# Performance work log

Measured on AMD Instinct MI355X. Metric: run time of the kernel, lower is better.

## Reference

```python
import jax, jax.numpy as jnp
import numpy as np

N_NODES = 32
GAT_OUT = 64
LSTM_H = 128
N_CLS = 4
NEG_SLOPE = 0.2


def setup_inputs() -> dict:
    key = jax.random.key(0)
    ks = jax.random.split(key, 12)
    B, T, E = 32, 512, 96
    F, H = GAT_OUT, LSTM_H
    s = 0.05
    return {
        "x_seq": jax.random.normal(ks[0], (B, T, N_NODES), jnp.float32),
        "edge_index": jax.random.randint(ks[1], (2, E), 0, N_NODES, jnp.int32),
        # GATConv params (heads=1): lin weight [in=1, F], attention vectors [F], bias [F]
        "w_gat": jax.random.normal(ks[2], (1, F), jnp.float32) * s,
        "att_src": jax.random.normal(ks[3], (F,), jnp.float32) * s,
        "att_dst": jax.random.normal(ks[4], (F,), jnp.float32) * s,
        "b_gat": jnp.zeros((F,), jnp.float32),
        # LSTM params, torch gate order (i, f, g, o)
        "W_ih": jax.random.normal(ks[5], (N_NODES * F, 4 * H), jnp.float32) * s,
        "W_hh": jax.random.normal(ks[6], (H, 4 * H), jnp.float32) * s,
        "b_ih": jnp.zeros((4 * H,), jnp.float32),
        "b_hh": jnp.zeros((4 * H,), jnp.float32),
        # classifier
        "W_fc": jax.random.normal(ks[7], (H, N_CLS), jnp.float32) * s,
        "b_fc": jnp.zeros((N_CLS,), jnp.float32),
    }


def _forward(x_seq, edge_index, w_gat, att_src, att_dst, b_gat,
             W_ih, W_hh, b_ih, b_hh, W_fc, b_fc):
    B, T, N = x_seq.shape
    F = w_gat.shape[1]
    H = W_hh.shape[0]

    # --- GAT over all (B,T) steps at once (PyG GATConv, heads=1, self-loops) ---
    loops = jnp.arange(N, dtype=edge_index.dtype)
    src = jnp.concatenate([edge_index[0], loops])  # [Et]
    dst = jnp.concatenate([edge_index[1], loops])  # [Et]
    Et = src.shape[0]

    h = x_seq[..., None] * w_gat            # [B,T,N,F] (in_channels=1 linear)
    a_s = h @ att_src                        # [B,T,N]
    a_d = h @ att_dst                        # [B,T,N]
    e = a_s[..., src] + a_d[..., dst]        # [B,T,Et]
    e = jnp.where(e > 0, e, NEG_SLOPE * e)   # LeakyReLU(0.2)

    # segment softmax over destination node, batched over B*T
    e2 = jnp.moveaxis(e, -1, 0).reshape(Et, B * T)
    m = jax.ops.segment_max(e2, dst, num_segments=N)        # [N,B*T]
    ex = jnp.exp(e2 - m[dst])
    z = jax.ops.segment_sum(ex, dst, num_segments=N)        # [N,B*T]
    alpha = ex / z[dst]                                      # [Et,B*T]
    alpha = jnp.moveaxis(alpha.reshape(Et, B, T), 0, -1)     # [B,T,Et]

    msg = alpha[..., None] * h[:, :, src, :]                 # [B,T,Et,F]
    onehot = (dst[:, None] == jnp.arange(N)).astype(h.dtype)  # [Et,N]
    out = jnp.einsum('btef,en->btnf', msg, onehot) + b_gat    # [B,T,N,F]

    seq = out.reshape(B, T, N * F)           # [B,T,2048]

    # --- single-layer LSTM (batch_first), torch gate order i,f,g,o ---
    xw = seq @ W_ih + (b_ih + b_hh)          # [B,T,4H]

    def step(carry, xw_t):
        hs, cs = carry
        g = xw_t + hs @ W_hh                 # [B,4H]
        i, f, gg, o = jnp.split(g, 4, axis=-1)
        cs = jax.nn.sigmoid(f) * cs + jax.nn.sigmoid(i) * jnp.tanh(gg)
        hs = jax.nn.sigmoid(o) * jnp.tanh(cs)
        return (hs, cs), None

    h0 = jnp.zeros((B, H), seq.dtype)
    (h_last, _), _ = jax.lax.scan(step, (h0, h0), jnp.moveaxis(xw, 1, 0))

    return h_last @ W_fc + b_fc              # [B,num_classes]


def reference(x_seq, edge_index, w_gat, att_src, att_dst, b_gat,
              W_ih, W_hh, b_ih, b_hh, W_fc, b_fc):
    return _forward(x_seq, edge_index, w_gat, att_src, att_dst, b_gat,
                    W_ih, W_hh, b_ih, b_hh, W_fc, b_fc)
```

## Files before the change

kernel.cpp:

```cpp
#include <hip/hip_runtime.h>
#include <hip/hip_fp16.h>

#define NN 32
#define FF 64
#define HH 128
#define G4 512
#define BB 32
#define TT 512
#define ET 128
#define NPOS (BB*TT)
#define POSB 32

__device__ __forceinline__ float frcp(float x) { return __builtin_amdgcn_rcpf(x); }

__global__ __launch_bounds__(512) void prep_kernel(const float* __restrict__ w_gat,
                                                   const float* __restrict__ b_gat,
                                                   const float* __restrict__ W_ih,
                                                   const float* __restrict__ W_hh,
                                                   float* __restrict__ W_eff,
                                                   float* __restrict__ biasp,
                                                   float* __restrict__ Wt) {
  int j = threadIdx.x;
  int n = blockIdx.x;
  float accw = 0.f, accb = 0.f;
#pragma unroll 8
  for (int f = 0; f < FF; ++f) {
    float wv = W_ih[(n * FF + f) * G4 + j];
    accw = fmaf(w_gat[f], wv, accw);
    accb = fmaf(b_gat[f], wv, accb);
  }
  W_eff[n * G4 + j] = accw;
  biasp[n * G4 + j] = accb;
  __half* Wt16 = (__half*)Wt;
  int g0 = (n * G4 + j) * 4;
#pragma unroll
  for (int qq = 0; qq < 4; ++qq) {
    int E = g0 + qq;
    int tl = E >> 7;
    int idx = E & 127;
    int frag = idx >> 3;
    int e = idx & 7;
    int g = frag >> 2, q = frag & 3;
    int w = tl >> 6, l = tl & 63;
    int k = q * 32 + ((l >> 4) * 8) + e;
    int col = g * 128 + w * 16 + (l & 15);
    Wt16[E] = __float2half(W_hh[k * G4 + col]);
  }
}

__global__ __launch_bounds__(256) void gatxw_kernel(const float* __restrict__ x_seq,
                                                    const int* __restrict__ ei,
                                                    const float* __restrict__ w_gat,
                                                    const float* __restrict__ att_src,
                                                    const float* __restrict__ att_dst,
                                                    const float* __restrict__ b_ih,
                                                    const float* __restrict__ b_hh,
                                                    const float* __restrict__ W_eff,
                                                    const float* __restrict__ biasp,
                                                    float* __restrict__ xw) {
  __shared__ int srt[ET];
  __shared__ int offs[NN + 1];
  __shared__ int cnt[NN];
  __shared__ float xs[POSB * NN];
  __shared__ float sl[POSB * NN];
  __shared__ float scal_sh[2];
  int tid = threadIdx.x;
  int posbase = blockIdx.x * POSB;
  float we0[NN], we1[NN];
#pragma unroll
  for (int nn = 0; nn < NN; ++nn) {
    we0[nn] = W_eff[nn * G4 + tid];
    we1[nn] = W_eff[nn * G4 + 256 + tid];
  }
  float b0 = b_ih[tid] + b_hh[tid];
  float b1 = b_ih[256 + tid] + b_hh[256 + tid];
#pragma unroll 8
  for (int n = 0; n < NN; ++n) {
    b0 += biasp[n * G4 + tid];
    b1 += biasp[n * G4 + 256 + tid];
  }
  if (tid < NN) cnt[tid] = 0;
  __syncthreads();
  int es = 0, ed = 0, tk = 0;
  if (tid < ET) {
    if (tid < 96) { es = ei[tid]; ed = ei[96 + tid]; }
    else { es = tid - 96; ed = tid - 96; }
    tk = atomicAdd(&cnt[ed], 1);
  }
  __syncthreads();
  if (tid == 0) {
    offs[0] = 0;
    for (int n = 0; n < NN; ++n) offs[n + 1] = offs[n] + cnt[n];
  }
  if (tid == 1) {
    float cs = 0.f, cd = 0.f;
    for (int f = 0; f < FF; ++f) {
      cs = fmaf(w_gat[f], att_src[f], cs);
      cd = fmaf(w_gat[f], att_dst[f], cd);
    }
    scal_sh[0] = cs;
    scal_sh[1] = cd;
  }
  __syncthreads();
  if (tid < ET) srt[offs[ed] + tk] = es;
#pragma unroll
  for (int c = 0; c < POSB * NN / 256; ++c)
    xs[c * 256 + tid] = x_seq[posbase * NN + c * 256 + tid];
  __syncthreads();
  float cs = scal_sh[0], cd = scal_sh[1];
  int n = tid & 31;
  int e0 = offs[n], e1 = offs[n + 1];
#pragma unroll
  for (int pb = 0; pb < POSB / 8; ++pb) {
    int p = pb * 8 + (tid >> 5);
    int base = p * 32;
    float xn = xs[base + n];
    float cdxn = cd * xn;
    float m = -3.0e38f;
    for (int e = e0; e < e1; ++e) {
      float ev = fmaf(cs, xs[base + srt[e]], cdxn);
      ev = ev > 0.f ? ev : 0.2f * ev;
      m = fmaxf(m, ev);
    }
    float z = 0.f, sa = 0.f;
    for (int e = e0; e < e1; ++e) {
      float xsv = xs[base + srt[e]];
      float ev = fmaf(cs, xsv, cdxn);
      ev = ev > 0.f ? ev : 0.2f * ev;
      float ex = __expf(ev - m);
      z += ex;
      sa = fmaf(ex, xsv, sa);
    }
    sl[base + n] = sa * frcp(z);
  }
  __syncthreads();
#pragma unroll 4
  for (int pp = 0; pp < POSB; ++pp) {
    const float4* sp = (const float4*)&sl[pp * 32];
    float a0 = b0, a1 = b1;
#pragma unroll
    for (int q = 0; q < 8; ++q) {
      float4 sv = sp[q];
      a0 = fmaf(sv.x, we0[4 * q], a0);
      a0 = fmaf(sv.y, we0[4 * q + 1], a0);
      a0 = fmaf(sv.z, we0[4 * q + 2], a0);
      a0 = fmaf(sv.w, we0[4 * q + 3], a0);
      a1 = fmaf(sv.x, we1[4 * q], a1);
      a1 = fmaf(sv.y, we1[4 * q + 1], a1);
      a1 = fmaf(sv.z, we1[4 * q + 2], a1);
      a1 = fmaf(sv.w, we1[4 * q + 3], a1);
    }
    size_t row = (size_t)(posbase + pp) * G4;
    xw[row + tid] = a0;
    xw[row + 256 + tid] = a1;
  }
}


#define MFMA_Q(AQ, BI, BF, BG, BO) \
  "v_mfma_f32_16x16x32_f16 v[216:219], v[" AQ "], v[" BI "], v[216:219]\n\t" \
  "v_mfma_f32_16x16x32_f16 v[220:223], v[" AQ "], v[" BF "], v[220:223]\n\t" \
  "v_mfma_f32_16x16x32_f16 v[224:227], v[" AQ "], v[" BG "], v[224:227]\n\t" \
  "v_mfma_f32_16x16x32_f16 v[228:231], v[" AQ "], v[" BO "], v[228:231]\n\t"

#define PHASE(X0, X1, X2, X3, RD, WR) \
  "s_waitcnt vmcnt(4)\n\t" \
  "v_mov_b32 v216, " X0 "\n\t" \
  "v_mov_b32 v220, " X1 "\n\t" \
  "v_mov_b32 v224, " X2 "\n\t" \
  "v_mov_b32 v228, " X3 "\n\t" \
  "ds_read_b128 v[32:35], " RD "\n\t" \
  "ds_read_b128 v[36:39], " RD " offset:64\n\t" \
  "ds_read_b128 v[40:43], " RD " offset:128\n\t" \
  "ds_read_b128 v[44:47], " RD " offset:192\n\t" \
  "s_waitcnt lgkmcnt(3)\n\t" \
  MFMA_Q("32:35", "64:67",   "80:83",   "96:99",   "112:115") \
  "s_waitcnt lgkmcnt(2)\n\t" \
  MFMA_Q("36:39", "68:71",   "84:87",   "100:103", "116:119") \
  "s_waitcnt lgkmcnt(1)\n\t" \
  MFMA_Q("40:43", "72:75",   "88:91",   "104:107", "120:123") \
  "s_waitcnt lgkmcnt(0)\n\t" \
  MFMA_Q("44:47", "76:79",   "92:95",   "108:111", "124:127") \
  "global_load_dword " X0 ", v194, %[xwb]\n\t" \
  "global_load_dword " X1 ", v194, %[xwb] offset:512\n\t" \
  "global_load_dword " X2 ", v194, %[xwb] offset:1024\n\t" \
  "global_load_dword " X3 ", v194, %[xwb] offset:1536\n\t" \
  "v_add_u32 v194, 0x800, v194\n\t" \
  "s_nop 7\n\t" \
  "s_nop 7\n\t" \
  "v_mul_f32 v204, v200, v216\n\t" \
  "v_mul_f32 v205, v200, v220\n\t" \
  "v_mul_f32 v206, v201, v224\n\t" \
  "v_mul_f32 v207, v200, v228\n\t" \
  "v_exp_f32 v204, v204\n\t" \
  "v_exp_f32 v205, v205\n\t" \
  "v_exp_f32 v206, v206\n\t" \
  "v_exp_f32 v207, v207\n\t" \
  "v_add_f32 v204, 1.0, v204\n\t" \
  "v_add_f32 v205, 1.0, v205\n\t" \
  "v_add_f32 v206, 1.0, v206\n\t" \
  "v_add_f32 v207, 1.0, v207\n\t" \
  "v_rcp_f32 v204, v204\n\t" \
  "v_rcp_f32 v205, v205\n\t" \
  "v_rcp_f32 v206, v206\n\t" \
  "v_rcp_f32 v207, v207\n\t" \
  "v_fma_f32 v206, -2.0, v206, 1.0\n\t" \
  "v_mul_f32 v210, v204, v206\n\t" \
  "v_fma_f32 v199, v205, v199, v210\n\t" \
  "v_mul_f32 v211, v201, v199\n\t" \
  "v_exp_f32 v211, v211\n\t" \
  "s_nop 0\n\t" \
  "v_add_f32 v211, 1.0, v211\n\t" \
  "v_rcp_f32 v211, v211\n\t" \
  "s_nop 0\n\t" \
  "v_fma_f32 v211, -2.0, v211, 1.0\n\t" \
  "v_mul_f32 v211, v207, v211\n\t" \
  "v_cvt_f16_f32 v211, v211\n\t" \
  "ds_write_b16 " WR ", v211\n\t" \
  "s_waitcnt lgkmcnt(0)\n\t" \
  "s_barrier\n\t"

__global__ __launch_bounds__(512, 2) void lstm_kernel(const float* __restrict__ xw,
                                                      const float* __restrict__ Wt,
                                                      const float* __restrict__ W_fc,
                                                      const float* __restrict__ b_fc,
                                                      float* __restrict__ out) {
  __shared__ __align__(16) float hlds[128];
  int b = blockIdx.x, tid = threadIdx.x;
  int w = tid >> 6, l = tid & 63;
  int u = w * 16 + (l & 15);
  if (tid < 128) hlds[tid] = 0.f;
  const float* xwb = xw + (size_t)b * TT * G4;
  unsigned xoff0 = (unsigned)(u * 4);
  unsigned wtoff = (unsigned)(tid * 256);
  unsigned lbase = (unsigned)(uintptr_t)&hlds[0];
  unsigned rda = lbase + (unsigned)((l >> 4) * 16);
  unsigned rdb = rda + 256;
  unsigned wra = lbase + (unsigned)(u * 2);
  unsigned wrb = wra + 256;
  __syncthreads();
  asm volatile(
    "v_mov_b32 v194, %[xo]\n\t"
    "v_mov_b32 v195, %[rda]\n\t"
    "v_mov_b32 v196, %[rdb]\n\t"
    "v_mov_b32 v197, %[wra]\n\t"
    "v_mov_b32 v198, %[wrb]\n\t"
    "v_mov_b32 v199, 0\n\t"
    "v_mov_b32 v200, 0xbfb8aa3b\n\t"
    "v_mov_b32 v201, 0x4038aa3b\n\t"
    "v_mov_b32 v217, 0\n\t" "v_mov_b32 v218, 0\n\t" "v_mov_b32 v219, 0\n\t"
    "v_mov_b32 v221, 0\n\t" "v_mov_b32 v222, 0\n\t" "v_mov_b32 v223, 0\n\t"
    "v_mov_b32 v225, 0\n\t" "v_mov_b32 v226, 0\n\t" "v_mov_b32 v227, 0\n\t"
    "v_mov_b32 v229, 0\n\t" "v_mov_b32 v230, 0\n\t" "v_mov_b32 v231, 0\n\t"
    "global_load_dword v240, v194, %[xwb]\n\t"
    "global_load_dword v241, v194, %[xwb] offset:512\n\t"
    "global_load_dword v242, v194, %[xwb] offset:1024\n\t"
    "global_load_dword v243, v194, %[xwb] offset:1536\n\t"
    "v_add_u32 v194, 0x800, v194\n\t"
    "global_load_dword v244, v194, %[xwb]\n\t"
    "global_load_dword v245, v194, %[xwb] offset:512\n\t"
    "global_load_dword v246, v194, %[xwb] offset:1024\n\t"
    "global_load_dword v247, v194, %[xwb] offset:1536\n\t"
    "v_add_u32 v194, 0x800, v194\n\t"
    "global_load_dwordx4 v[64:67], %[wto], %[wtb] offset:0\n\t"
    "global_load_dwordx4 v[68:71], %[wto], %[wtb] offset:16\n\t"
    "global_load_dwordx4 v[72:75], %[wto], %[wtb] offset:32\n\t"
    "global_load_dwordx4 v[76:79], %[wto], %[wtb] offset:48\n\t"
    "global_load_dwordx4 v[80:83], %[wto], %[wtb] offset:64\n\t"
    "global_load_dwordx4 v[84:87], %[wto], %[wtb] offset:80\n\t"
    "global_load_dwordx4 v[88:91], %[wto], %[wtb] offset:96\n\t"
    "global_load_dwordx4 v[92:95], %[wto], %[wtb] offset:112\n\t"
    "global_load_dwordx4 v[96:99], %[wto], %[wtb] offset:128\n\t"
    "global_load_dwordx4 v[100:103], %[wto], %[wtb] offset:144\n\t"
    "global_load_dwordx4 v[104:107], %[wto], %[wtb] offset:160\n\t"
    "global_load_dwordx4 v[108:111], %[wto], %[wtb] offset:176\n\t"
    "global_load_dwordx4 v[112:115], %[wto], %[wtb] offset:192\n\t"
    "global_load_dwordx4 v[116:119], %[wto], %[wtb] offset:208\n\t"
    "global_load_dwordx4 v[120:123], %[wto], %[wtb] offset:224\n\t"
    "global_load_dwordx4 v[124:127], %[wto], %[wtb] offset:240\n\t"
    "s_waitcnt vmcnt(0)\n\t"
    "s_movk_i32 s20, 0x100\n\t"
    "L_lstm_%=:\n\t"
    PHASE("v240", "v241", "v242", "v243", "v195", "v198")
    PHASE("v244", "v245", "v246", "v247", "v196", "v197")
    "s_sub_u32 s20, s20, 1\n\t"
    "s_cmp_lg_u32 s20, 0\n\t"
    "s_cbranch_scc1 L_lstm_%=\n\t"
    "s_waitcnt vmcnt(0) lgkmcnt(0)\n\t"
    :
    : [xwb]"s"(xwb), [wtb]"s"(Wt), [wto]"v"(wtoff), [xo]"v"(xoff0),
      [rda]"v"(rda), [rdb]"v"(rdb), [wra]"v"(wra), [wrb]"v"(wrb)
    : "memory", "scc", "s20",
      "v32","v33","v34","v35","v36","v37","v38","v39",
      "v40","v41","v42","v43","v44","v45","v46","v47",
      "v64","v65","v66","v67","v68","v69","v70","v71",
      "v72","v73","v74","v75","v76","v77","v78","v79",
      "v80","v81","v82","v83","v84","v85","v86","v87",
      "v88","v89","v90","v91","v92","v93","v94","v95",
      "v96","v97","v98","v99","v100","v101","v102","v103",
      "v104","v105","v106","v107","v108","v109","v110","v111",
      "v112","v113","v114","v115","v116","v117","v118","v119",
      "v120","v121","v122","v123","v124","v125","v126","v127",
      "v194","v195","v196","v197","v198","v199","v200","v201",
      "v204","v205","v206","v207","v208","v209","v210","v211",
      "v216","v217","v218","v219","v220","v221","v222","v223",
      "v224","v225","v226","v227","v228","v229","v230","v231",
      "v240","v241","v242","v243","v244","v245","v246","v247");
  __syncthreads();
  if (tid < 4) {
    const __half* hf = (const __half*)hlds;
    float acc = b_fc[tid];
#pragma unroll 8
    for (int k = 0; k < HH; ++k)
      acc = fmaf(__half2float(hf[k]), W_fc[k * 4 + tid], acc);
    out[b * 4 + tid] = acc;
  }
}

extern "C" void kernel_launch(void* const* d_in, const int* in_sizes, int n_in,
                              void* d_out, int out_size, void* d_ws, size_t ws_size,
                              hipStream_t stream) {
  const float* x_seq   = (const float*)d_in[0];
  const int*   ei      = (const int*)d_in[1];
  const float* w_gat   = (const float*)d_in[2];
  const float* att_src = (const float*)d_in[3];
  const float* att_dst = (const float*)d_in[4];
  const float* b_gat   = (const float*)d_in[5];
  const float* W_ih    = (const float*)d_in[6];
  const float* W_hh    = (const float*)d_in[7];
  const float* b_ih    = (const float*)d_in[8];
  const float* b_hh    = (const float*)d_in[9];
  const float* W_fc    = (const float*)d_in[10];
  const float* b_fc    = (const float*)d_in[11];

  float* ws = (float*)d_ws;
  float* Wt    = ws;
  float* xw    = Wt + 65536;
  float* W_eff = xw + (size_t)(NPOS + 8) * G4;
  float* biasp = W_eff + NN * G4;

  prep_kernel<<<NN, G4, 0, stream>>>(w_gat, b_gat, W_ih, W_hh, W_eff, biasp, Wt);
  gatxw_kernel<<<NPOS / POSB, 256, 0, stream>>>(x_seq, ei, w_gat, att_src, att_dst,
                                                b_ih, b_hh, W_eff, biasp, xw);
  lstm_kernel<<<BB, G4, 0, stream>>>(xw, Wt, W_fc, b_fc, (float*)d_out);
}
```

Measured before the change: 335.8 us.

## Fuse input projection into LSTM MFMA loop, stream fp16 GAT outputs

The GAT kernel now writes only the 32 per-node attention-aggregated scalars per position in fp16, dropping the 32-to-512 input projection and the large fp32 xw buffer. The LSTM kernel loads W_eff fragments and the combined bias into registers once, then adds one extra MFMA group per step that multiplies the streamed 32-wide fp16 input by W_eff. This removes the big xw write and read round trip to memory, at the cost of an extra MFMA on the serial recurrence path and fp16 rounding of the inputs and W_eff.

```diff
diff --git a/kernel.cpp b/kernel.cpp
--- a/kernel.cpp
+++ b/kernel.cpp
@@ -53,32 +53,14 @@
                                                     const float* __restrict__ w_gat,
                                                     const float* __restrict__ att_src,
                                                     const float* __restrict__ att_dst,
-                                                    const float* __restrict__ b_ih,
-                                                    const float* __restrict__ b_hh,
-                                                    const float* __restrict__ W_eff,
-                                                    const float* __restrict__ biasp,
-                                                    float* __restrict__ xw) {
+                                                    __half* __restrict__ sl16) {
   __shared__ int srt[ET];
   __shared__ int offs[NN + 1];
   __shared__ int cnt[NN];
   __shared__ float xs[POSB * NN];
-  __shared__ float sl[POSB * NN];
   __shared__ float scal_sh[2];
   int tid = threadIdx.x;
   int posbase = blockIdx.x * POSB;
-  float we0[NN], we1[NN];
-#pragma unroll
-  for (int nn = 0; nn < NN; ++nn) {
-    we0[nn] = W_eff[nn * G4 + tid];
-    we1[nn] = W_eff[nn * G4 + 256 + tid];
-  }
-  float b0 = b_ih[tid] + b_hh[tid];
-  float b1 = b_ih[256 + tid] + b_hh[256 + tid];
-#pragma unroll 8
-  for (int n = 0; n < NN; ++n) {
-    b0 += biasp[n * G4 + tid];
-    b1 += biasp[n * G4 + 256 + tid];
-  }
   if (tid < NN) cnt[tid] = 0;
   __syncthreads();
   int es = 0, ed = 0, tk = 0;
@@ -131,28 +113,7 @@
       z += ex;
       sa = fmaf(ex, xsv, sa);
     }
-    sl[base + n] = sa * frcp(z);
-  }
-  __syncthreads();
-#pragma unroll 4
-  for (int pp = 0; pp < POSB; ++pp) {
-    const float4* sp = (const float4*)&sl[pp * 32];
-    float a0 = b0, a1 = b1;
-#pragma unroll
-    for (int q = 0; q < 8; ++q) {
-      float4 sv = sp[q];
-      a0 = fmaf(sv.x, we0[4 * q], a0);
-      a0 = fmaf(sv.y, we0[4 * q + 1], a0);
-      a0 = fmaf(sv.z, we0[4 * q + 2], a0);
-      a0 = fmaf(sv.w, we0[4 * q + 3], a0);
-      a1 = fmaf(sv.x, we1[4 * q], a1);
-      a1 = fmaf(sv.y, we1[4 * q + 1], a1);
-      a1 = fmaf(sv.z, we1[4 * q + 2], a1);
-      a1 = fmaf(sv.w, we1[4 * q + 3], a1);
-    }
-    size_t row = (size_t)(posbase + pp) * G4;
-    xw[row + tid] = a0;
-    xw[row + 256 + tid] = a1;
+    sl16[(size_t)(posbase + p) * 32 + n] = __float2half(sa * frcp(z));
   }
 }
 
@@ -163,16 +124,17 @@
   "v_mfma_f32_16x16x32_f16 v[224:227], v[" AQ "], v[" BG "], v[224:227]\n\t" \
   "v_mfma_f32_16x16x32_f16 v[228:231], v[" AQ "], v[" BO "], v[228:231]\n\t"
 
-#define PHASE(X0, X1, X2, X3, RD, WR) \
-  "s_waitcnt vmcnt(4)\n\t" \
-  "v_mov_b32 v216, " X0 "\n\t" \
-  "v_mov_b32 v220, " X1 "\n\t" \
-  "v_mov_b32 v224, " X2 "\n\t" \
-  "v_mov_b32 v228, " X3 "\n\t" \
+#define PHASE(SLQ, RD, WR) \
+  "s_waitcnt vmcnt(1)\n\t" \
+  "v_mov_b32 v216, v232\n\t" \
+  "v_mov_b32 v220, v233\n\t" \
+  "v_mov_b32 v224, v234\n\t" \
+  "v_mov_b32 v228, v235\n\t" \
   "ds_read_b128 v[32:35], " RD "\n\t" \
   "ds_read_b128 v[36:39], " RD " offset:64\n\t" \
   "ds_read_b128 v[40:43], " RD " offset:128\n\t" \
   "ds_read_b128 v[44:47], " RD " offset:192\n\t" \
+  MFMA_Q(SLQ, "128:131", "132:135", "136:139", "140:143") \
   "s_waitcnt lgkmcnt(3)\n\t" \
   MFMA_Q("32:35", "64:67",   "80:83",   "96:99",   "112:115") \
   "s_waitcnt lgkmcnt(2)\n\t" \
@@ -181,11 +143,8 @@
   MFMA_Q("40:43", "72:75",   "88:91",   "104:107", "120:123") \
   "s_waitcnt lgkmcnt(0)\n\t" \
   MFMA_Q("44:47", "76:79",   "92:95",   "108:111", "124:127") \
-  "global_load_dword " X0 ", v194, %[xwb]\n\t" \
-  "global_load_dword " X1 ", v194, %[xwb] offset:512\n\t" \
-  "global_load_dword " X2 ", v194, %[xwb] offset:1024\n\t" \
-  "global_load_dword " X3 ", v194, %[xwb] offset:1536\n\t" \
-  "v_add_u32 v194, 0x800, v194\n\t" \
+  "global_load_dwordx4 v[" SLQ "], v194, %[slb]\n\t" \
+  "v_add_u32 v194, 64, v194\n\t" \
   "s_nop 7\n\t" \
   "s_nop 7\n\t" \
   "v_mul_f32 v204, v200, v216\n\t" \
@@ -220,21 +179,46 @@
   "s_waitcnt lgkmcnt(0)\n\t" \
   "s_barrier\n\t"
 
-__global__ __launch_bounds__(512, 2) void lstm_kernel(const float* __restrict__ xw,
+__global__ __launch_bounds__(512, 2) void lstm_kernel(const __half* __restrict__ sl16,
                                                       const float* __restrict__ Wt,
+                                                      const float* __restrict__ W_eff,
+                                                      const float* __restrict__ biasp,
+                                                      const float* __restrict__ b_ih,
+                                                      const float* __restrict__ b_hh,
                                                       const float* __restrict__ W_fc,
                                                       const float* __restrict__ b_fc,
                                                       float* __restrict__ out) {
-  __shared__ __align__(16) float hlds[128];
+  __shared__ __align__(16) float shm[128 + 10240];
+  float* hlds = shm;
   int b = blockIdx.x, tid = threadIdx.x;
   int w = tid >> 6, l = tid & 63;
   int u = w * 16 + (l & 15);
+  int kc = (l >> 4) * 8;
+  {
+    unsigned* tp = (unsigned*)&shm[128];
+    int base = tid * 20;
+#pragma unroll
+    for (int g = 0; g < 4; ++g) {
+      int col = g * 128 + u;
+      float bb = b_ih[col] + b_hh[col];
+#pragma unroll 8
+      for (int n = 0; n < NN; ++n) bb += biasp[n * G4 + col];
+#pragma unroll
+      for (int j = 0; j < 4; ++j) {
+        unsigned lo = (unsigned)__half_as_ushort(__float2half(W_eff[(kc + 2 * j) * G4 + col]));
+        unsigned hi = (unsigned)__half_as_ushort(__float2half(W_eff[(kc + 2 * j + 1) * G4 + col]));
+        tp[base + g * 4 + j] = lo | (hi << 16);
+      }
+      tp[base + 16 + g] = __float_as_uint(bb);
+    }
+  }
   if (tid < 128) hlds[tid] = 0.f;
-  const float* xwb = xw + (size_t)b * TT * G4;
-  unsigned xoff0 = (unsigned)(u * 4);
+  const __half* slb = sl16 + (size_t)b * TT * 32;
+  unsigned xoff0 = (unsigned)(kc * 2);
   unsigned wtoff = (unsigned)(tid * 256);
-  unsigned lbase = (unsigned)(uintptr_t)&hlds[0];
-  unsigned rda = lbase + (unsigned)((l >> 4) * 16);
+  unsigned lbase = (unsigned)(uintptr_t)&shm[0];
+  unsigned tmpoff = lbase + 512u + (unsigned)(tid * 80);
+  unsigned rda = lbase + (unsigned)(kc * 2);
   unsigned rdb = rda + 256;
   unsigned wra = lbase + (unsigned)(u * 2);
   unsigned wrb = wra + 256;
@@ -248,20 +232,20 @@
     "v_mov_b32 v199, 0\n\t"
     "v_mov_b32 v200, 0xbfb8aa3b\n\t"
     "v_mov_b32 v201, 0x4038aa3b\n\t"
+    "v_mov_b32 v203, %[tmp]\n\t"
     "v_mov_b32 v217, 0\n\t" "v_mov_b32 v218, 0\n\t" "v_mov_b32 v219, 0\n\t"
     "v_mov_b32 v221, 0\n\t" "v_mov_b32 v222, 0\n\t" "v_mov_b32 v223, 0\n\t"
     "v_mov_b32 v225, 0\n\t" "v_mov_b32 v226, 0\n\t" "v_mov_b32 v227, 0\n\t"
     "v_mov_b32 v229, 0\n\t" "v_mov_b32 v230, 0\n\t" "v_mov_b32 v231, 0\n\t"
-    "global_load_dword v240, v194, %[xwb]\n\t"
-    "global_load_dword v241, v194, %[xwb] offset:512\n\t"
-    "global_load_dword v242, v194, %[xwb] offset:1024\n\t"
-    "global_load_dword v243, v194, %[xwb] offset:1536\n\t"
-    "v_add_u32 v194, 0x800, v194\n\t"
-    "global_load_dword v244, v194, %[xwb]\n\t"
-    "global_load_dword v245, v194, %[xwb] offset:512\n\t"
-    "global_load_dword v246, v194, %[xwb] offset:1024\n\t"
-    "global_load_dword v247, v194, %[xwb] offset:1536\n\t"
-    "v_add_u32 v194, 0x800, v194\n\t"
+    "ds_read_b128 v[128:131], v203\n\t"
+    "ds_read_b128 v[132:135], v203 offset:16\n\t"
+    "ds_read_b128 v[136:139], v203 offset:32\n\t"
+    "ds_read_b128 v[140:143], v203 offset:48\n\t"
+    "ds_read_b128 v[232:235], v203 offset:64\n\t"
+    "global_load_dwordx4 v[240:243], v194, %[slb]\n\t"
+    "v_add_u32 v194, 64, v194\n\t"
+    "global_load_dwordx4 v[244:247], v194, %[slb]\n\t"
+    "v_add_u32 v194, 64, v194\n\t"
     "global_load_dwordx4 v[64:67], %[wto], %[wtb] offset:0\n\t"
     "global_load_dwordx4 v[68:71], %[wto], %[wtb] offset:16\n\t"
     "global_load_dwordx4 v[72:75], %[wto], %[wtb] offset:32\n\t"
@@ -278,18 +262,18 @@
     "global_load_dwordx4 v[116:119], %[wto], %[wtb] offset:208\n\t"
     "global_load_dwordx4 v[120:123], %[wto], %[wtb] offset:224\n\t"
     "global_load_dwordx4 v[124:127], %[wto], %[wtb] offset:240\n\t"
-    "s_waitcnt vmcnt(0)\n\t"
+    "s_waitcnt vmcnt(0) lgkmcnt(0)\n\t"
     "s_movk_i32 s20, 0x100\n\t"
     "L_lstm_%=:\n\t"
-    PHASE("v240", "v241", "v242", "v243", "v195", "v198")
-    PHASE("v244", "v245", "v246", "v247", "v196", "v197")
+    PHASE("240:243", "v195", "v198")
+    PHASE("244:247", "v196", "v197")
     "s_sub_u32 s20, s20, 1\n\t"
     "s_cmp_lg_u32 s20, 0\n\t"
     "s_cbranch_scc1 L_lstm_%=\n\t"
     "s_waitcnt vmcnt(0) lgkmcnt(0)\n\t"
     :
-    : [xwb]"s"(xwb), [wtb]"s"(Wt), [wto]"v"(wtoff), [xo]"v"(xoff0),
-      [rda]"v"(rda), [rdb]"v"(rdb), [wra]"v"(wra), [wrb]"v"(wrb)
+    : [slb]"s"(slb), [wtb]"s"(Wt), [wto]"v"(wtoff), [xo]"v"(xoff0),
+      [rda]"v"(rda), [rdb]"v"(rdb), [wra]"v"(wra), [wrb]"v"(wrb), [tmp]"v"(tmpoff)
     : "memory", "scc", "s20",
       "v32","v33","v34","v35","v36","v37","v38","v39",
       "v40","v41","v42","v43","v44","v45","v46","v47",
@@ -301,10 +285,13 @@
       "v104","v105","v106","v107","v108","v109","v110","v111",
       "v112","v113","v114","v115","v116","v117","v118","v119",
       "v120","v121","v122","v123","v124","v125","v126","v127",
+      "v128","v129","v130","v131","v132","v133","v134","v135",
+      "v136","v137","v138","v139","v140","v141","v142","v143",
       "v194","v195","v196","v197","v198","v199","v200","v201",
-      "v204","v205","v206","v207","v208","v209","v210","v211",
-      "v216","v217","v218","v219","v220","v221","v222","v223",
-      "v224","v225","v226","v227","v228","v229","v230","v231",
+      "v202","v203","v204","v205","v206","v207","v208","v209",
+      "v210","v211","v216","v217","v218","v219","v220","v221",
+      "v222","v223","v224","v225","v226","v227","v228","v229",
+      "v230","v231","v232","v233","v234","v235",
       "v240","v241","v242","v243","v244","v245","v246","v247");
   __syncthreads();
   if (tid < 4) {
@@ -335,12 +322,12 @@
 
   float* ws = (float*)d_ws;
   float* Wt    = ws;
-  float* xw    = Wt + 65536;
-  float* W_eff = xw + (size_t)(NPOS + 8) * G4;
+  __half* sl16 = (__half*)(ws + 65536);
+  float* W_eff = ws + 65536 + 262400;
   float* biasp = W_eff + NN * G4;
 
   prep_kernel<<<NN, G4, 0, stream>>>(w_gat, b_gat, W_ih, W_hh, W_eff, biasp, Wt);
-  gatxw_kernel<<<NPOS / POSB, 256, 0, stream>>>(x_seq, ei, w_gat, att_src, att_dst,
-                                                b_ih, b_hh, W_eff, biasp, xw);
-  lstm_kernel<<<BB, G4, 0, stream>>>(xw, Wt, W_fc, b_fc, (float*)d_out);
+  gatxw_kernel<<<NPOS / POSB, 256, 0, stream>>>(x_seq, ei, w_gat, att_src, att_dst, sl16);
+  lstm_kernel<<<BB, G4, 0, stream>>>(sl16, Wt, W_eff, biasp, b_ih, b_hh, W_fc, b_fc,
+                                     (float*)d_out);
 }
```

Measured after the change: 345.5 us. +2.9%, slower.

## Halve LSTM block to 4 waves, each computing two hidden-unit tiles per step

Applied to the files above, without the earlier changes.

Each LSTM wave now owns 32 hidden units, two 16-wide MFMA tiles per gate, so the recurrent kernel runs with 256 threads instead of 512. The W_hh fragment layout in prep is re-permuted so each thread holds twice as many fp16 weight registers, and the per-step xw loads and gate math are doubled per thread. The goal is to cut barrier and LDS synchronisation cost per timestep, since fewer waves participate in each s_barrier. The cost is longer serial MFMA and transcendental chains per wave and much higher VGPR use.

```diff
diff --git a/kernel.cpp b/kernel.cpp
--- a/kernel.cpp
+++ b/kernel.cpp
@@ -36,14 +36,14 @@
 #pragma unroll
   for (int qq = 0; qq < 4; ++qq) {
     int E = g0 + qq;
-    int tl = E >> 7;
-    int idx = E & 127;
-    int frag = idx >> 3;
+    int tl = E >> 8;
+    int idx = E & 255;
+    int ft = idx >> 3;
     int e = idx & 7;
-    int g = frag >> 2, q = frag & 3;
+    int tt = ft >> 4, g = (ft >> 2) & 3, q = ft & 3;
     int w = tl >> 6, l = tl & 63;
     int k = q * 32 + ((l >> 4) * 8) + e;
-    int col = g * 128 + w * 16 + (l & 15);
+    int col = g * 128 + w * 32 + tt * 16 + (l & 15);
     Wt16[E] = __float2half(W_hh[k * G4 + col]);
   }
 }
@@ -157,70 +157,107 @@
 }
 
 
-#define MFMA_Q(AQ, BI, BF, BG, BO) \
-  "v_mfma_f32_16x16x32_f16 v[216:219], v[" AQ "], v[" BI "], v[216:219]\n\t" \
-  "v_mfma_f32_16x16x32_f16 v[220:223], v[" AQ "], v[" BF "], v[220:223]\n\t" \
-  "v_mfma_f32_16x16x32_f16 v[224:227], v[" AQ "], v[" BG "], v[224:227]\n\t" \
-  "v_mfma_f32_16x16x32_f16 v[228:231], v[" AQ "], v[" BO "], v[228:231]\n\t"
-
-#define PHASE(X0, X1, X2, X3, RD, WR) \
-  "s_waitcnt vmcnt(4)\n\t" \
-  "v_mov_b32 v216, " X0 "\n\t" \
-  "v_mov_b32 v220, " X1 "\n\t" \
-  "v_mov_b32 v224, " X2 "\n\t" \
-  "v_mov_b32 v228, " X3 "\n\t" \
+#define MQ8(AQ, B0, B1, B2, B3, B4, B5, B6, B7) \
+  "v_mfma_f32_16x16x32_f16 v[192:195], v[" AQ "], v[" B0 "], v[192:195]\n\t" \
+  "v_mfma_f32_16x16x32_f16 v[196:199], v[" AQ "], v[" B1 "], v[196:199]\n\t" \
+  "v_mfma_f32_16x16x32_f16 v[200:203], v[" AQ "], v[" B2 "], v[200:203]\n\t" \
+  "v_mfma_f32_16x16x32_f16 v[204:207], v[" AQ "], v[" B3 "], v[204:207]\n\t" \
+  "v_mfma_f32_16x16x32_f16 v[208:211], v[" AQ "], v[" B4 "], v[208:211]\n\t" \
+  "v_mfma_f32_16x16x32_f16 v[212:215], v[" AQ "], v[" B5 "], v[212:215]\n\t" \
+  "v_mfma_f32_16x16x32_f16 v[216:219], v[" AQ "], v[" B6 "], v[216:219]\n\t" \
+  "v_mfma_f32_16x16x32_f16 v[220:223], v[" AQ "], v[" B7 "], v[220:223]\n\t"
+
+#define PHASE(X0, X1, X2, X3, X4, X5, X6, X7, RD, WR) \
+  "s_waitcnt vmcnt(8)\n\t" \
+  "v_mov_b32 v192, " X0 "\n\t" \
+  "v_mov_b32 v196, " X1 "\n\t" \
+  "v_mov_b32 v200, " X2 "\n\t" \
+  "v_mov_b32 v204, " X3 "\n\t" \
+  "v_mov_b32 v208, " X4 "\n\t" \
+  "v_mov_b32 v212, " X5 "\n\t" \
+  "v_mov_b32 v216, " X6 "\n\t" \
+  "v_mov_b32 v220, " X7 "\n\t" \
   "ds_read_b128 v[32:35], " RD "\n\t" \
   "ds_read_b128 v[36:39], " RD " offset:64\n\t" \
   "ds_read_b128 v[40:43], " RD " offset:128\n\t" \
   "ds_read_b128 v[44:47], " RD " offset:192\n\t" \
   "s_waitcnt lgkmcnt(3)\n\t" \
-  MFMA_Q("32:35", "64:67",   "80:83",   "96:99",   "112:115") \
+  MQ8("32:35", "64:67",  "80:83",  "96:99",   "112:115", "128:131", "144:147", "160:163", "176:179") \
   "s_waitcnt lgkmcnt(2)\n\t" \
-  MFMA_Q("36:39", "68:71",   "84:87",   "100:103", "116:119") \
+  MQ8("36:39", "68:71",  "84:87",  "100:103", "116:119", "132:135", "148:151", "164:167", "180:183") \
   "s_waitcnt lgkmcnt(1)\n\t" \
-  MFMA_Q("40:43", "72:75",   "88:91",   "104:107", "120:123") \
+  MQ8("40:43", "72:75",  "88:91",  "104:107", "120:123", "136:139", "152:155", "168:171", "184:187") \
   "s_waitcnt lgkmcnt(0)\n\t" \
-  MFMA_Q("44:47", "76:79",   "92:95",   "108:111", "124:127") \
-  "global_load_dword " X0 ", v194, %[xwb]\n\t" \
-  "global_load_dword " X1 ", v194, %[xwb] offset:512\n\t" \
-  "global_load_dword " X2 ", v194, %[xwb] offset:1024\n\t" \
-  "global_load_dword " X3 ", v194, %[xwb] offset:1536\n\t" \
-  "v_add_u32 v194, 0x800, v194\n\t" \
+  MQ8("44:47", "76:79",  "92:95",  "108:111", "124:127", "140:143", "156:159", "172:175", "188:191") \
+  "global_load_dword " X0 ", v48, %[xwb]\n\t" \
+  "global_load_dword " X1 ", v48, %[xwb] offset:512\n\t" \
+  "global_load_dword " X2 ", v48, %[xwb] offset:1024\n\t" \
+  "global_load_dword " X3 ", v48, %[xwb] offset:1536\n\t" \
+  "global_load_dword " X4 ", v48, %[xwb] offset:64\n\t" \
+  "global_load_dword " X5 ", v48, %[xwb] offset:576\n\t" \
+  "global_load_dword " X6 ", v48, %[xwb] offset:1088\n\t" \
+  "global_load_dword " X7 ", v48, %[xwb] offset:1600\n\t" \
+  "v_add_u32 v48, 0x800, v48\n\t" \
   "s_nop 7\n\t" \
   "s_nop 7\n\t" \
-  "v_mul_f32 v204, v200, v216\n\t" \
-  "v_mul_f32 v205, v200, v220\n\t" \
-  "v_mul_f32 v206, v201, v224\n\t" \
-  "v_mul_f32 v207, v200, v228\n\t" \
-  "v_exp_f32 v204, v204\n\t" \
-  "v_exp_f32 v205, v205\n\t" \
-  "v_exp_f32 v206, v206\n\t" \
-  "v_exp_f32 v207, v207\n\t" \
-  "v_add_f32 v204, 1.0, v204\n\t" \
-  "v_add_f32 v205, 1.0, v205\n\t" \
-  "v_add_f32 v206, 1.0, v206\n\t" \
-  "v_add_f32 v207, 1.0, v207\n\t" \
-  "v_rcp_f32 v204, v204\n\t" \
-  "v_rcp_f32 v205, v205\n\t" \
-  "v_rcp_f32 v206, v206\n\t" \
-  "v_rcp_f32 v207, v207\n\t" \
-  "v_fma_f32 v206, -2.0, v206, 1.0\n\t" \
-  "v_mul_f32 v210, v204, v206\n\t" \
-  "v_fma_f32 v199, v205, v199, v210\n\t" \
-  "v_mul_f32 v211, v201, v199\n\t" \
-  "v_exp_f32 v211, v211\n\t" \
-  "s_nop 0\n\t" \
-  "v_add_f32 v211, 1.0, v211\n\t" \
-  "v_rcp_f32 v211, v211\n\t" \
-  "s_nop 0\n\t" \
-  "v_fma_f32 v211, -2.0, v211, 1.0\n\t" \
-  "v_mul_f32 v211, v207, v211\n\t" \
-  "v_cvt_f16_f32 v211, v211\n\t" \
-  "ds_write_b16 " WR ", v211\n\t" \
+  "v_mul_f32 v240, v55, v192\n\t" \
+  "v_mul_f32 v241, v55, v196\n\t" \
+  "v_mul_f32 v242, v56, v200\n\t" \
+  "v_mul_f32 v243, v55, v204\n\t" \
+  "v_mul_f32 v244, v55, v208\n\t" \
+  "v_mul_f32 v245, v55, v212\n\t" \
+  "v_mul_f32 v246, v56, v216\n\t" \
+  "v_mul_f32 v247, v55, v220\n\t" \
+  "v_exp_f32 v240, v240\n\t" \
+  "v_exp_f32 v241, v241\n\t" \
+  "v_exp_f32 v242, v242\n\t" \
+  "v_exp_f32 v243, v243\n\t" \
+  "v_exp_f32 v244, v244\n\t" \
+  "v_exp_f32 v245, v245\n\t" \
+  "v_exp_f32 v246, v246\n\t" \
+  "v_exp_f32 v247, v247\n\t" \
+  "v_add_f32 v240, 1.0, v240\n\t" \
+  "v_add_f32 v241, 1.0, v241\n\t" \
+  "v_add_f32 v242, 1.0, v242\n\t" \
+  "v_add_f32 v243, 1.0, v243\n\t" \
+  "v_add_f32 v244, 1.0, v244\n\t" \
+  "v_add_f32 v245, 1.0, v245\n\t" \
+  "v_add_f32 v246, 1.0, v246\n\t" \
+  "v_add_f32 v247, 1.0, v247\n\t" \
+  "v_rcp_f32 v240, v240\n\t" \
+  "v_rcp_f32 v241, v241\n\t" \
+  "v_rcp_f32 v242, v242\n\t" \
+  "v_rcp_f32 v243, v243\n\t" \
+  "v_rcp_f32 v244, v244\n\t" \
+  "v_rcp_f32 v245, v245\n\t" \
+  "v_rcp_f32 v246, v246\n\t" \
+  "v_rcp_f32 v247, v247\n\t" \
+  "v_fma_f32 v242, -2.0, v242, 1.0\n\t" \
+  "v_fma_f32 v246, -2.0, v246, 1.0\n\t" \
+  "v_mul_f32 v248, v240, v242\n\t" \
+  "v_mul_f32 v249, v244, v246\n\t" \
+  "v_fma_f32 v53, v241, v53, v248\n\t" \
+  "v_fma_f32 v54, v245, v54, v249\n\t" \
+  "v_mul_f32 v250, v56, v53\n\t" \
+  "v_mul_f32 v251, v56, v54\n\t" \
+  "v_exp_f32 v250, v250\n\t" \
+  "v_exp_f32 v251, v251\n\t" \
+  "v_add_f32 v250, 1.0, v250\n\t" \
+  "v_add_f32 v251, 1.0, v251\n\t" \
+  "v_rcp_f32 v250, v250\n\t" \
+  "v_rcp_f32 v251, v251\n\t" \
+  "v_fma_f32 v250, -2.0, v250, 1.0\n\t" \
+  "v_fma_f32 v251, -2.0, v251, 1.0\n\t" \
+  "v_mul_f32 v250, v243, v250\n\t" \
+  "v_mul_f32 v251, v247, v251\n\t" \
+  "v_cvt_f16_f32 v250, v250\n\t" \
+  "v_cvt_f16_f32 v251, v251\n\t" \
+  "ds_write_b16 " WR ", v250\n\t" \
+  "ds_write_b16 " WR ", v251 offset:32\n\t" \
   "s_waitcnt lgkmcnt(0)\n\t" \
   "s_barrier\n\t"
 
-__global__ __launch_bounds__(512, 2) void lstm_kernel(const float* __restrict__ xw,
+__global__ __launch_bounds__(256, 1) void lstm_kernel(const float* __restrict__ xw,
                                                       const float* __restrict__ Wt,
                                                       const float* __restrict__ W_fc,
                                                       const float* __restrict__ b_fc,
@@ -228,40 +265,53 @@
   __shared__ __align__(16) float hlds[128];
   int b = blockIdx.x, tid = threadIdx.x;
   int w = tid >> 6, l = tid & 63;
-  int u = w * 16 + (l & 15);
+  int u0 = w * 32 + (l & 15);
   if (tid < 128) hlds[tid] = 0.f;
   const float* xwb = xw + (size_t)b * TT * G4;
-  unsigned xoff0 = (unsigned)(u * 4);
-  unsigned wtoff = (unsigned)(tid * 256);
+  unsigned xoff0 = (unsigned)(u0 * 4);
+  unsigned wtoff = (unsigned)(tid * 512);
   unsigned lbase = (unsigned)(uintptr_t)&hlds[0];
   unsigned rda = lbase + (unsigned)((l >> 4) * 16);
   unsigned rdb = rda + 256;
-  unsigned wra = lbase + (unsigned)(u * 2);
+  unsigned wra = lbase + (unsigned)(u0 * 2);
   unsigned wrb = wra + 256;
   __syncthreads();
   asm volatile(
-    "v_mov_b32 v194, %[xo]\n\t"
-    "v_mov_b32 v195, %[rda]\n\t"
-    "v_mov_b32 v196, %[rdb]\n\t"
-    "v_mov_b32 v197, %[wra]\n\t"
-    "v_mov_b32 v198, %[wrb]\n\t"
-    "v_mov_b32 v199, 0\n\t"
-    "v_mov_b32 v200, 0xbfb8aa3b\n\t"
-    "v_mov_b32 v201, 0x4038aa3b\n\t"
+    "v_mov_b32 v48, %[xo]\n\t"
+    "v_mov_b32 v49, %[rda]\n\t"
+    "v_mov_b32 v50, %[rdb]\n\t"
+    "v_mov_b32 v51, %[wra]\n\t"
+    "v_mov_b32 v52, %[wrb]\n\t"
+    "v_mov_b32 v53, 0\n\t"
+    "v_mov_b32 v54, 0\n\t"
+    "v_mov_b32 v55, 0xbfb8aa3b\n\t"
+    "v_mov_b32 v56, 0x4038aa3b\n\t"
+    "v_mov_b32 v193, 0\n\t" "v_mov_b32 v194, 0\n\t" "v_mov_b32 v195, 0\n\t"
+    "v_mov_b32 v197, 0\n\t" "v_mov_b32 v198, 0\n\t" "v_mov_b32 v199, 0\n\t"
+    "v_mov_b32 v201, 0\n\t" "v_mov_b32 v202, 0\n\t" "v_mov_b32 v203, 0\n\t"
+    "v_mov_b32 v205, 0\n\t" "v_mov_b32 v206, 0\n\t" "v_mov_b32 v207, 0\n\t"
+    "v_mov_b32 v209, 0\n\t" "v_mov_b32 v210, 0\n\t" "v_mov_b32 v211, 0\n\t"
+    "v_mov_b32 v213, 0\n\t" "v_mov_b32 v214, 0\n\t" "v_mov_b32 v215, 0\n\t"
     "v_mov_b32 v217, 0\n\t" "v_mov_b32 v218, 0\n\t" "v_mov_b32 v219, 0\n\t"
     "v_mov_b32 v221, 0\n\t" "v_mov_b32 v222, 0\n\t" "v_mov_b32 v223, 0\n\t"
-    "v_mov_b32 v225, 0\n\t" "v_mov_b32 v226, 0\n\t" "v_mov_b32 v227, 0\n\t"
-    "v_mov_b32 v229, 0\n\t" "v_mov_b32 v230, 0\n\t" "v_mov_b32 v231, 0\n\t"
-    "global_load_dword v240, v194, %[xwb]\n\t"
-    "global_load_dword v241, v194, %[xwb] offset:512\n\t"
-    "global_load_dword v242, v194, %[xwb] offset:1024\n\t"
-    "global_load_dword v243, v194, %[xwb] offset:1536\n\t"
-    "v_add_u32 v194, 0x800, v194\n\t"
-    "global_load_dword v244, v194, %[xwb]\n\t"
-    "global_load_dword v245, v194, %[xwb] offset:512\n\t"
-    "global_load_dword v246, v194, %[xwb] offset:1024\n\t"
-    "global_load_dword v247, v194, %[xwb] offset:1536\n\t"
-    "v_add_u32 v194, 0x800, v194\n\t"
+    "global_load_dword v224, v48, %[xwb]\n\t"
+    "global_load_dword v225, v48, %[xwb] offset:512\n\t"
+    "global_load_dword v226, v48, %[xwb] offset:1024\n\t"
+    "global_load_dword v227, v48, %[xwb] offset:1536\n\t"
+    "global_load_dword v228, v48, %[xwb] offset:64\n\t"
+    "global_load_dword v229, v48, %[xwb] offset:576\n\t"
+    "global_load_dword v230, v48, %[xwb] offset:1088\n\t"
+    "global_load_dword v231, v48, %[xwb] offset:1600\n\t"
+    "v_add_u32 v48, 0x800, v48\n\t"
+    "global_load_dword v232, v48, %[xwb]\n\t"
+    "global_load_dword v233, v48, %[xwb] offset:512\n\t"
+    "global_load_dword v234, v48, %[xwb] offset:1024\n\t"
+    "global_load_dword v235, v48, %[xwb] offset:1536\n\t"
+    "global_load_dword v236, v48, %[xwb] offset:64\n\t"
+    "global_load_dword v237, v48, %[xwb] offset:576\n\t"
+    "global_load_dword v238, v48, %[xwb] offset:1088\n\t"
+    "global_load_dword v239, v48, %[xwb] offset:1600\n\t"
+    "v_add_u32 v48, 0x800, v48\n\t"
     "global_load_dwordx4 v[64:67], %[wto], %[wtb] offset:0\n\t"
     "global_load_dwordx4 v[68:71], %[wto], %[wtb] offset:16\n\t"
     "global_load_dwordx4 v[72:75], %[wto], %[wtb] offset:32\n\t"
@@ -278,11 +328,27 @@
     "global_load_dwordx4 v[116:119], %[wto], %[wtb] offset:208\n\t"
     "global_load_dwordx4 v[120:123], %[wto], %[wtb] offset:224\n\t"
     "global_load_dwordx4 v[124:127], %[wto], %[wtb] offset:240\n\t"
+    "global_load_dwordx4 v[128:131], %[wto], %[wtb] offset:256\n\t"
+    "global_load_dwordx4 v[132:135], %[wto], %[wtb] offset:272\n\t"
+    "global_load_dwordx4 v[136:139], %[wto], %[wtb] offset:288\n\t"
+    "global_load_dwordx4 v[140:143], %[wto], %[wtb] offset:304\n\t"
+    "global_load_dwordx4 v[144:147], %[wto], %[wtb] offset:320\n\t"
+    "global_load_dwordx4 v[148:151], %[wto], %[wtb] offset:336\n\t"
+    "global_load_dwordx4 v[152:155], %[wto], %[wtb] offset:352\n\t"
+    "global_load_dwordx4 v[156:159], %[wto], %[wtb] offset:368\n\t"
+    "global_load_dwordx4 v[160:163], %[wto], %[wtb] offset:384\n\t"
+    "global_load_dwordx4 v[164:167], %[wto], %[wtb] offset:400\n\t"
+    "global_load_dwordx4 v[168:171], %[wto], %[wtb] offset:416\n\t"
+    "global_load_dwordx4 v[172:175], %[wto], %[wtb] offset:432\n\t"
+    "global_load_dwordx4 v[176:179], %[wto], %[wtb] offset:448\n\t"
+    "global_load_dwordx4 v[180:183], %[wto], %[wtb] offset:464\n\t"
+    "global_load_dwordx4 v[184:187], %[wto], %[wtb] offset:480\n\t"
+    "global_load_dwordx4 v[188:191], %[wto], %[wtb] offset:496\n\t"
     "s_waitcnt vmcnt(0)\n\t"
     "s_movk_i32 s20, 0x100\n\t"
     "L_lstm_%=:\n\t"
-    PHASE("v240", "v241", "v242", "v243", "v195", "v198")
-    PHASE("v244", "v245", "v246", "v247", "v196", "v197")
+    PHASE("v224", "v225", "v226", "v227", "v228", "v229", "v230", "v231", "v49", "v52")
+    PHASE("v232", "v233", "v234", "v235", "v236", "v237", "v238", "v239", "v50", "v51")
     "s_sub_u32 s20, s20, 1\n\t"
     "s_cmp_lg_u32 s20, 0\n\t"
     "s_cbranch_scc1 L_lstm_%=\n\t"
@@ -293,6 +359,7 @@
     : "memory", "scc", "s20",
       "v32","v33","v34","v35","v36","v37","v38","v39",
       "v40","v41","v42","v43","v44","v45","v46","v47",
+      "v48","v49","v50","v51","v52","v53","v54","v55","v56",
       "v64","v65","v66","v67","v68","v69","v70","v71",
       "v72","v73","v74","v75","v76","v77","v78","v79",
       "v80","v81","v82","v83","v84","v85","v86","v87",
@@ -301,11 +368,22 @@
       "v104","v105","v106","v107","v108","v109","v110","v111",
       "v112","v113","v114","v115","v116","v117","v118","v119",
       "v120","v121","v122","v123","v124","v125","v126","v127",
-      "v194","v195","v196","v197","v198","v199","v200","v201",
-      "v204","v205","v206","v207","v208","v209","v210","v211",
+      "v128","v129","v130","v131","v132","v133","v134","v135",
+      "v136","v137","v138","v139","v140","v141","v142","v143",
+      "v144","v145","v146","v147","v148","v149","v150","v151",
+      "v152","v153","v154","v155","v156","v157","v158","v159",
+      "v160","v161","v162","v163","v164","v165","v166","v167",
+      "v168","v169","v170","v171","v172","v173","v174","v175",
+      "v176","v177","v178","v179","v180","v181","v182","v183",
+      "v184","v185","v186","v187","v188","v189","v190","v191",
+      "v192","v193","v194","v195","v196","v197","v198","v199",
+      "v200","v201","v202","v203","v204","v205","v206","v207",
+      "v208","v209","v210","v211","v212","v213","v214","v215",
       "v216","v217","v218","v219","v220","v221","v222","v223",
       "v224","v225","v226","v227","v228","v229","v230","v231",
-      "v240","v241","v242","v243","v244","v245","v246","v247");
+      "v232","v233","v234","v235","v236","v237","v238","v239",
+      "v240","v241","v242","v243","v244","v245","v246","v247",
+      "v248","v249","v250","v251");
   __syncthreads();
   if (tid < 4) {
     const __half* hf = (const __half*)hlds;
@@ -342,5 +420,5 @@
   prep_kernel<<<NN, G4, 0, stream>>>(w_gat, b_gat, W_ih, W_hh, W_eff, biasp, Wt);
   gatxw_kernel<<<NPOS / POSB, 256, 0, stream>>>(x_seq, ei, w_gat, att_src, att_dst,
                                                 b_ih, b_hh, W_eff, biasp, xw);
-  lstm_kernel<<<BB, G4, 0, stream>>>(xw, Wt, W_fc, b_fc, (float*)d_out);
+  lstm_kernel<<<BB, 256, 0, stream>>>(xw, Wt, W_fc, b_fc, (float*)d_out);
 }
```

Measured after the change: 392.6 us. 16.9% more time.
